# Kernel tuning notes

Hardware: AMD Instinct MI355X
Metric: run time of the kernel (lower is better)

The kernel has to match this reference:

```python
import jax, jax.numpy as jnp
import numpy as np

DIM = 16          # matrix is DIM x DIM -> E = DIM*DIM independent MLPs
E = DIM * DIM
D_IN = DIM - 1    # each MLP input size
H = 128           # hidden nodes
B = 8192          # batch size


def setup_inputs() -> dict:
    key = jax.random.key(0)
    ks = jax.random.split(key, 7)
    x_batch = jax.random.normal(ks[0], (B, D_IN), dtype=jnp.float32)
    # Batched parameters for the E independent MLPs (Linear init ~ U(-1/sqrt(fan_in), ...) approximated by scaled normal)
    W1 = jax.random.normal(ks[1], (E, D_IN, H), dtype=jnp.float32) / np.sqrt(D_IN)
    b1 = jax.random.normal(ks[2], (E, H), dtype=jnp.float32) / np.sqrt(D_IN)
    W2 = jax.random.normal(ks[3], (E, H, H), dtype=jnp.float32) / np.sqrt(H)
    b2 = jax.random.normal(ks[4], (E, H), dtype=jnp.float32) / np.sqrt(H)
    W3 = jax.random.normal(ks[5], (E, H, 1), dtype=jnp.float32) / np.sqrt(H)
    b3 = jax.random.normal(ks[6], (E, 1), dtype=jnp.float32) / np.sqrt(H)
    return {"x_batch": x_batch, "W1": W1, "b1": b1, "W2": W2, "b2": b2, "W3": W3, "b3": b3}


def reference(x_batch, W1, b1, W2, b2, W3, b3):
    # All E tiny MLPs evaluated as batched (grouped) GEMMs over the expert axis e.
    # h1: [E, B, H]
    h1 = jax.nn.sigmoid(jnp.einsum('bi,eih->ebh', x_batch, W1) + b1[:, None, :])
    # h2: [E, B, H]
    h2 = jax.nn.sigmoid(jnp.einsum('ebh,ehk->ebk', h1, W2) + b2[:, None, :])
    # out_e: [E, B] scalar output per MLP
    out_e = jnp.einsum('ebh,eho->ebo', h2, W3)[..., 0] + b3[:, None, 0]
    # torch.stack(entries, 1).view(B, dim, dim): entry e goes to flat position e of a [B, E] tensor
    return out_e.T.reshape(x_batch.shape[0], DIM, DIM)
```

## Files before the change

kernel.cpp:

```cpp
#include <hip/hip_runtime.h>
#include <hip/hip_bf16.h>

#define E_CNT  256
#define D_IN   15
#define HDIM   128
#define BATCH  8192
#define NPAIR  256
#define NL2E   -1.44269504088896341f

typedef float f32x4 __attribute__((ext_vector_type(4)));
typedef short bf16x8 __attribute__((ext_vector_type(8)));
typedef unsigned int uint4v __attribute__((ext_vector_type(4)));

#define MFMA16(a, b, c) __builtin_amdgcn_mfma_f32_16x16x32_bf16((a), (b), (c), 0, 0, 0)
#define SCHED_FENCE() __builtin_amdgcn_sched_barrier(0)

static __device__ inline unsigned short f2bf_rnd(float f) {
    unsigned u = __builtin_bit_cast(unsigned, f);
    return (unsigned short)((u + 0x8000u) >> 16);
}

static __device__ inline float sg(float az) {
    float e = __builtin_amdgcn_exp2f(az);
    return __builtin_amdgcn_rcpf(1.0f + e);
}

static __device__ inline unsigned pack2(float lo, float hi_) {
    unsigned a = __builtin_bit_cast(unsigned, lo) + 0x8000u;
    unsigned b = __builtin_bit_cast(unsigned, hi_) + 0x8000u;
#if __has_builtin(__builtin_amdgcn_perm)
    return __builtin_amdgcn_perm(b, a, 0x07060302u);
#else
    return (a >> 16) | (b & 0xffff0000u);
#endif
}

static __device__ inline void pl32swap(unsigned &a, unsigned &b) {
#if __has_builtin(__builtin_amdgcn_permlane32_swap)
    auto r = __builtin_amdgcn_permlane32_swap(a, b, false, false);
    a = (unsigned)r[0];
    b = (unsigned)r[1];
#else
    asm volatile("v_permlane32_swap_b32 %0, %1" : "+v"(a), "+v"(b));
#endif
}

static __device__ inline void pl16swap(unsigned &a, unsigned &b) {
#if __has_builtin(__builtin_amdgcn_permlane16_swap)
    auto r = __builtin_amdgcn_permlane16_swap(a, b, false, false);
    a = (unsigned)r[0];
    b = (unsigned)r[1];
#else
    asm volatile("v_permlane16_swap_b32 %0, %1" : "+v"(a), "+v"(b));
#endif
}

static __device__ inline f32x4 zero4() { f32x4 z = {0.f, 0.f, 0.f, 0.f}; return z; }

static __device__ inline bf16x8 mk_bfrag(unsigned X0, unsigned X1, unsigned Y0, unsigned Y1) {
    pl32swap(X0, Y0);
    pl32swap(X1, Y1);
    pl16swap(X0, Y0);
    pl16swap(X1, Y1);
    uint4v u = {X0, X1, Y0, Y1};
    return __builtin_bit_cast(bf16x8, u);
}

__global__ __launch_bounds__(256)
void prep_x_kernel(const float* __restrict__ x, unsigned short* __restrict__ xbf)
{
    int i = blockIdx.x * 256 + threadIdx.x;
    if (i >= BATCH * 16) return;
    int row = i >> 4, k = i & 15;
    float v = (k < D_IN) ? x[row * D_IN + k] : 1.0f;
    xbf[i] = f2bf_rnd(v);
}

__global__ __launch_bounds__(256, 3)
void mlp256_kernel(const float* __restrict__ x, const unsigned short* __restrict__ xbf,
                   const float* __restrict__ W1, const float* __restrict__ b1,
                   const float* __restrict__ W2, const float* __restrict__ b2,
                   const float* __restrict__ W3, const float* __restrict__ b3,
                   float* __restrict__ dst, int use_xbf, int transposed)
{
    __shared__ __align__(16) unsigned short w2f[32 * 512];
    __shared__ __align__(16) unsigned short w1f[8 * 512];
    __shared__ __align__(16) unsigned short b2f[8 * 512];
    __shared__ __align__(16) unsigned short w3f[4 * 512];

    const int tid  = threadIdx.x;
    const int wave = tid >> 6;
    const int lane = tid & 63;
    const int l15  = lane & 15;
    const int q    = lane >> 4;

    const int bid = blockIdx.x;
    const int e   = bid & 255;
    const int rg  = bid >> 8;

    const float* w1p = W1 + e * (D_IN * HDIM);
    const float* b1p = b1 + e * HDIM;
    const float* w2p = W2 + e * (HDIM * HDIM);
    const float* b2p = b2 + e * HDIM;
    const float* w3p = W3 + e * HDIM;
    const float  b3v = b3[e];

    for (int i = tid; i < HDIM * HDIM; i += 256) {
        int h = i & 127, k = i >> 7;
        int t = ((h >> 4) << 2) + (k >> 5);
        int ln = (((k >> 3) & 3) << 4) + (h & 15);
        w2f[t * 512 + ln * 8 + (k & 7)] = f2bf_rnd(w2p[k * HDIM + h] * NL2E);
    }
    for (int i = tid; i < HDIM * 32; i += 256) {
        int h = i & 127, k = i >> 7;
        float v = (k < D_IN) ? w1p[k * HDIM + h] * NL2E
                : (k == D_IN) ? b1p[h] * NL2E : 0.0f;
        int t = h >> 4;
        int ln = (((k >> 3) & 3) << 4) + (h & 15);
        w1f[t * 512 + ln * 8 + (k & 7)] = f2bf_rnd(v);
    }
    for (int i = tid; i < 8 * 512; i += 256) b2f[i] = 0;
    for (int i = tid; i < 4 * 512; i += 256) w3f[i] = 0;
    __syncthreads();
    if (tid < HDIM)
        b2f[(tid >> 4) * 512 + (tid & 15) * 8] = f2bf_rnd(b2p[tid] * NL2E);
    if (tid < HDIM)
        w3f[(tid >> 5) * 512 + (((tid >> 3) & 3) << 4) * 8 + (tid & 7)] = f2bf_rnd(w3p[tid]);

    bf16x8 ONEB;
#pragma unroll
    for (int j = 0; j < 8; ++j) ONEB[j] = 0;
    ONEB[0] = (short)0x3F80;

    __syncthreads();

    const unsigned short* w1B = w1f + lane * 8;
    const unsigned short* w2B = w2f + lane * 8;
    const unsigned short* b2B = b2f + lane * 8;
    const unsigned short* w3B = w3f + lane * 8;
    const int xoff = l15 * 16 + (q & 1) * 8;

    for (int p = rg + 3 * wave; p < NPAIR; p += 12) {
        const int cA = 2 * p, cB = 2 * p + 1;

        bf16x8 XA, XBv;
        if (use_xbf) {
            XA  = *reinterpret_cast<const bf16x8*>(xbf + (size_t)cA * 256 + xoff);
            XBv = *reinterpret_cast<const bf16x8*>(xbf + (size_t)cB * 256 + xoff);
        } else {
            const float* xa = x + (size_t)(cA * 16 + l15) * D_IN;
            const float* xb = x + (size_t)(cB * 16 + l15) * D_IN;
#pragma unroll
            for (int j = 0; j < 8; ++j) {
                int k = (q & 1) * 8 + j;
                XA[j]  = (short)f2bf_rnd((k < D_IN) ? xa[k] : 1.0f);
                XBv[j] = (short)f2bf_rnd((k < D_IN) ? xb[k] : 1.0f);
            }
        }

        bf16x8 H1A[4], H1B[4];
#pragma unroll
        for (int kb = 0; kb < 4; ++kb) {
            bf16x8 wa0 = *reinterpret_cast<const bf16x8*>(w1B + (2 * kb) * 512);
            f32x4 aa = MFMA16(wa0, XA,  zero4());
            f32x4 ba = MFMA16(wa0, XBv, zero4());
            bf16x8 wa1 = *reinterpret_cast<const bf16x8*>(w1B + (2 * kb + 1) * 512);
            f32x4 ab = MFMA16(wa1, XA,  zero4());
            f32x4 bb = MFMA16(wa1, XBv, zero4());
            unsigned pa0 = pack2(sg(aa[0]), sg(aa[1]));
            unsigned pa1 = pack2(sg(aa[2]), sg(aa[3]));
            unsigned pa2 = pack2(sg(ab[0]), sg(ab[1]));
            unsigned pa3 = pack2(sg(ab[2]), sg(ab[3]));
            H1A[kb] = mk_bfrag(pa0, pa1, pa2, pa3);
            unsigned pb0 = pack2(sg(ba[0]), sg(ba[1]));
            unsigned pb1 = pack2(sg(ba[2]), sg(ba[3]));
            unsigned pb2 = pack2(sg(bb[0]), sg(bb[1]));
            unsigned pb3 = pack2(sg(bb[2]), sg(bb[3]));
            H1B[kb] = mk_bfrag(pb0, pb1, pb2, pb3);
            SCHED_FENCE();
        }

        f32x4 o3A = zero4(), o3B = zero4();
#pragma unroll
        for (int pt = 0; pt < 4; ++pt) {
            unsigned qa0, qa1, qa2, qa3, qb0, qb1, qb2, qb3;
            {
                const int ot = 2 * pt;
                bf16x8 wb = *reinterpret_cast<const bf16x8*>(b2B + ot * 512);
                f32x4 cA2 = MFMA16(wb, ONEB, zero4());
                f32x4 cB2 = MFMA16(wb, ONEB, zero4());
#pragma unroll
                for (int kb = 0; kb < 4; ++kb) {
                    bf16x8 wa = *reinterpret_cast<const bf16x8*>(w2B + (ot * 4 + kb) * 512);
                    cA2 = MFMA16(wa, H1A[kb], cA2);
                    cB2 = MFMA16(wa, H1B[kb], cB2);
                }
                qa0 = pack2(sg(cA2[0]), sg(cA2[1]));
                qa1 = pack2(sg(cA2[2]), sg(cA2[3]));
                qb0 = pack2(sg(cB2[0]), sg(cB2[1]));
                qb1 = pack2(sg(cB2[2]), sg(cB2[3]));
            }
            SCHED_FENCE();
            {
                const int ot = 2 * pt + 1;
                bf16x8 wb = *reinterpret_cast<const bf16x8*>(b2B + ot * 512);
                f32x4 cA2 = MFMA16(wb, ONEB, zero4());
                f32x4 cB2 = MFMA16(wb, ONEB, zero4());
#pragma unroll
                for (int kb = 0; kb < 4; ++kb) {
                    bf16x8 wa = *reinterpret_cast<const bf16x8*>(w2B + (ot * 4 + kb) * 512);
                    cA2 = MFMA16(wa, H1A[kb], cA2);
                    cB2 = MFMA16(wa, H1B[kb], cB2);
                }
                qa2 = pack2(sg(cA2[0]), sg(cA2[1]));
                qa3 = pack2(sg(cA2[2]), sg(cA2[3]));
                qb2 = pack2(sg(cB2[0]), sg(cB2[1]));
                qb3 = pack2(sg(cB2[2]), sg(cB2[3]));
            }
            bf16x8 w3a = *reinterpret_cast<const bf16x8*>(w3B + pt * 512);
            bf16x8 H2A = mk_bfrag(qa0, qa1, qa2, qa3);
            o3A = MFMA16(w3a, H2A, o3A);
            bf16x8 H2B = mk_bfrag(qb0, qb1, qb2, qb3);
            o3B = MFMA16(w3a, H2B, o3B);
            SCHED_FENCE();
        }

        if (q == 0) {
            float vA = o3A[0] + b3v;
            float vB = o3B[0] + b3v;
            const int bbA = cA * 16 + l15;
            const int bbB = cB * 16 + l15;
            if (transposed) {
                dst[(size_t)e * BATCH + bbA] = vA;
                dst[(size_t)e * BATCH + bbB] = vB;
            } else {
                dst[(size_t)bbA * E_CNT + e] = vA;
                dst[(size_t)bbB * E_CNT + e] = vB;
            }
        }
    }
}

__global__ __launch_bounds__(256)
void transpose_out_kernel(const float* __restrict__ wsT, float* __restrict__ out)
{
    __shared__ float tile[64][65];
    const int tx = threadIdx.x & 63;
    const int ty = threadIdx.x >> 6;
    const int b0 = blockIdx.x * 64;
    const int e0 = blockIdx.y * 64;
#pragma unroll
    for (int r = ty; r < 64; r += 4)
        tile[r][tx] = wsT[(size_t)(e0 + r) * BATCH + b0 + tx];
    __syncthreads();
#pragma unroll
    for (int r = ty; r < 64; r += 4)
        out[(size_t)(b0 + r) * E_CNT + e0 + tx] = tile[tx][r];
}

extern "C" void kernel_launch(void* const* d_in, const int* in_sizes, int n_in,
                              void* d_out, int out_size, void* d_ws, size_t ws_size,
                              hipStream_t stream) {
    const float* x  = (const float*)d_in[0];
    const float* W1 = (const float*)d_in[1];
    const float* b1 = (const float*)d_in[2];
    const float* W2 = (const float*)d_in[3];
    const float* b2 = (const float*)d_in[4];
    const float* W3 = (const float*)d_in[5];
    const float* b3 = (const float*)d_in[6];
    float* out = (float*)d_out;

    const size_t XBF_BYTES = (size_t)BATCH * 16 * sizeof(unsigned short);
    const size_t WST_BYTES = (size_t)E_CNT * BATCH * sizeof(float);

    const bool have_xbf = ws_size >= XBF_BYTES + WST_BYTES;
    const bool have_wst = ws_size >= WST_BYTES;

    unsigned short* xbf = (unsigned short*)d_ws;
    float* wsT = have_xbf ? (float*)((char*)d_ws + XBF_BYTES) : (float*)d_ws;

    if (have_xbf)
        prep_x_kernel<<<dim3((BATCH * 16 + 255) / 256), dim3(256), 0, stream>>>(x, xbf);

    if (have_wst) {
        mlp256_kernel<<<dim3(E_CNT * 3), dim3(256), 0, stream>>>(
            x, xbf, W1, b1, W2, b2, W3, b3, wsT, have_xbf ? 1 : 0, 1);
        transpose_out_kernel<<<dim3(BATCH / 64, E_CNT / 64), dim3(256), 0, stream>>>(
            wsT, out);
    } else {
        mlp256_kernel<<<dim3(E_CNT * 3), dim3(256), 0, stream>>>(
            x, xbf, W1, b1, W2, b2, W3, b3, out, 0, 0);
    }
}
```

Baseline: 172.3 us.

## Compact LDS weight fragments to fit four blocks per CU with four blocks per expert

```diff
diff --git a/kernel.cpp b/kernel.cpp
--- a/kernel.cpp
+++ b/kernel.cpp
@@ -6,6 +6,7 @@
 #define HDIM   128
 #define BATCH  8192
 #define NPAIR  256
+#define BPE    4
 #define NL2E   -1.44269504088896341f
 
 typedef float f32x4 __attribute__((ext_vector_type(4)));
@@ -76,7 +77,7 @@
     xbf[i] = f2bf_rnd(v);
 }
 
-__global__ __launch_bounds__(256, 3)
+__global__ __launch_bounds__(256, 4)
 void mlp256_kernel(const float* __restrict__ x, const unsigned short* __restrict__ xbf,
                    const float* __restrict__ W1, const float* __restrict__ b1,
                    const float* __restrict__ W2, const float* __restrict__ b2,
@@ -84,9 +85,10 @@
                    float* __restrict__ dst, int use_xbf, int transposed)
 {
     __shared__ __align__(16) unsigned short w2f[32 * 512];
-    __shared__ __align__(16) unsigned short w1f[8 * 512];
-    __shared__ __align__(16) unsigned short b2f[8 * 512];
-    __shared__ __align__(16) unsigned short w3f[4 * 512];
+    __shared__ __align__(16) unsigned short w1f[8 * 256];
+    __shared__ __align__(16) unsigned short b2f[8 * 128];
+    __shared__ __align__(16) unsigned short w3f[128];
+    __shared__ __align__(16) unsigned short zb[8];
 
     const int tid  = threadIdx.x;
     const int wave = tid >> 6;
@@ -111,21 +113,18 @@
         int ln = (((k >> 3) & 3) << 4) + (h & 15);
         w2f[t * 512 + ln * 8 + (k & 7)] = f2bf_rnd(w2p[k * HDIM + h] * NL2E);
     }
-    for (int i = tid; i < HDIM * 32; i += 256) {
-        int h = i & 127, k = i >> 7;
-        float v = (k < D_IN) ? w1p[k * HDIM + h] * NL2E
-                : (k == D_IN) ? b1p[h] * NL2E : 0.0f;
-        int t = h >> 4;
-        int ln = (((k >> 3) & 3) << 4) + (h & 15);
-        w1f[t * 512 + ln * 8 + (k & 7)] = f2bf_rnd(v);
-    }
-    for (int i = tid; i < 8 * 512; i += 256) b2f[i] = 0;
-    for (int i = tid; i < 4 * 512; i += 256) w3f[i] = 0;
-    __syncthreads();
-    if (tid < HDIM)
-        b2f[(tid >> 4) * 512 + (tid & 15) * 8] = f2bf_rnd(b2p[tid] * NL2E);
-    if (tid < HDIM)
-        w3f[(tid >> 5) * 512 + (((tid >> 3) & 3) << 4) * 8 + (tid & 7)] = f2bf_rnd(w3p[tid]);
+    for (int i = tid; i < 8 * 256; i += 256) {
+        int t = i >> 8, ln = (i >> 3) & 31, j = i & 7;
+        int k = (ln >> 4) * 8 + j, h = t * 16 + (ln & 15);
+        float v = (k < D_IN) ? w1p[k * HDIM + h] : b1p[h];
+        w1f[i] = f2bf_rnd(v * NL2E);
+    }
+    for (int i = tid; i < 8 * 128; i += 256) {
+        int ot = i >> 7, l = (i >> 3) & 15, j = i & 7;
+        b2f[i] = (j == 0) ? f2bf_rnd(b2p[ot * 16 + l] * NL2E) : (unsigned short)0;
+    }
+    if (tid < 128) w3f[tid] = f2bf_rnd(w3p[tid]);
+    if (tid < 8)   zb[tid] = 0;
 
     bf16x8 ONEB;
 #pragma unroll
@@ -134,13 +133,16 @@
 
     __syncthreads();
 
-    const unsigned short* w1B = w1f + lane * 8;
+    const bool w1s = (lane < 32);
+    const bool b2s = (q == 0);
+    const bool w3s = (l15 == 0);
+    const unsigned short* w1D = w1f + lane * 8;
     const unsigned short* w2B = w2f + lane * 8;
-    const unsigned short* b2B = b2f + lane * 8;
-    const unsigned short* w3B = w3f + lane * 8;
+    const unsigned short* b2D = b2f + l15 * 8;
+    const unsigned short* w3D = w3f + q * 8;
     const int xoff = l15 * 16 + (q & 1) * 8;
 
-    for (int p = rg + 3 * wave; p < NPAIR; p += 12) {
+    for (int p = rg + 4 * wave; p < NPAIR; p += 16) {
         const int cA = 2 * p, cB = 2 * p + 1;
 
         bf16x8 XA, XBv;
@@ -161,10 +163,10 @@
         bf16x8 H1A[4], H1B[4];
 #pragma unroll
         for (int kb = 0; kb < 4; ++kb) {
-            bf16x8 wa0 = *reinterpret_cast<const bf16x8*>(w1B + (2 * kb) * 512);
+            bf16x8 wa0 = *reinterpret_cast<const bf16x8*>(w1s ? (w1D + (2 * kb) * 256) : zb);
             f32x4 aa = MFMA16(wa0, XA,  zero4());
             f32x4 ba = MFMA16(wa0, XBv, zero4());
-            bf16x8 wa1 = *reinterpret_cast<const bf16x8*>(w1B + (2 * kb + 1) * 512);
+            bf16x8 wa1 = *reinterpret_cast<const bf16x8*>(w1s ? (w1D + (2 * kb + 1) * 256) : zb);
             f32x4 ab = MFMA16(wa1, XA,  zero4());
             f32x4 bb = MFMA16(wa1, XBv, zero4());
             unsigned pa0 = pack2(sg(aa[0]), sg(aa[1]));
@@ -186,7 +188,7 @@
             unsigned qa0, qa1, qa2, qa3, qb0, qb1, qb2, qb3;
             {
                 const int ot = 2 * pt;
-                bf16x8 wb = *reinterpret_cast<const bf16x8*>(b2B + ot * 512);
+                bf16x8 wb = *reinterpret_cast<const bf16x8*>(b2s ? (b2D + ot * 128) : zb);
                 f32x4 cA2 = MFMA16(wb, ONEB, zero4());
                 f32x4 cB2 = MFMA16(wb, ONEB, zero4());
 #pragma unroll
@@ -203,7 +205,7 @@
             SCHED_FENCE();
             {
                 const int ot = 2 * pt + 1;
-                bf16x8 wb = *reinterpret_cast<const bf16x8*>(b2B + ot * 512);
+                bf16x8 wb = *reinterpret_cast<const bf16x8*>(b2s ? (b2D + ot * 128) : zb);
                 f32x4 cA2 = MFMA16(wb, ONEB, zero4());
                 f32x4 cB2 = MFMA16(wb, ONEB, zero4());
 #pragma unroll
@@ -217,7 +219,7 @@
                 qb2 = pack2(sg(cB2[0]), sg(cB2[1]));
                 qb3 = pack2(sg(cB2[2]), sg(cB2[3]));
             }
-            bf16x8 w3a = *reinterpret_cast<const bf16x8*>(w3B + pt * 512);
+            bf16x8 w3a = *reinterpret_cast<const bf16x8*>(w3s ? (w3D + pt * 32) : zb);
             bf16x8 H2A = mk_bfrag(qa0, qa1, qa2, qa3);
             o3A = MFMA16(w3a, H2A, o3A);
             bf16x8 H2B = mk_bfrag(qb0, qb1, qb2, qb3);
@@ -283,12 +285,12 @@
         prep_x_kernel<<<dim3((BATCH * 16 + 255) / 256), dim3(256), 0, stream>>>(x, xbf);
 
     if (have_wst) {
-        mlp256_kernel<<<dim3(E_CNT * 3), dim3(256), 0, stream>>>(
+        mlp256_kernel<<<dim3(E_CNT * BPE), dim3(256), 0, stream>>>(
             x, xbf, W1, b1, W2, b2, W3, b3, wsT, have_xbf ? 1 : 0, 1);
         transpose_out_kernel<<<dim3(BATCH / 64, E_CNT / 64), dim3(256), 0, stream>>>(
             wsT, out);
     } else {
-        mlp256_kernel<<<dim3(E_CNT * 3), dim3(256), 0, stream>>>(
+        mlp256_kernel<<<dim3(E_CNT * BPE), dim3(256), 0, stream>>>(
             x, xbf, W1, b1, W2, b2, W3, b3, out, 0, 0);
     }
 }
```

Result: faster. 166.8 us (-3.2%).
